# Optimization experiments

Measured on AMD Instinct MI355X. Metric: run time of the kernel, lower is better.

Reference implementation:

```python
import jax, jax.numpy as jnp
import numpy as np

K_SHARP = 10.0  # sigmoid sharpness from init kwarg k


def setup_inputs() -> dict:
    key = jax.random.key(0)
    k1, _ = jax.random.split(key)
    points = jax.random.normal(k1, (8192, 32), dtype=jnp.float32)
    # log-spaced thresholds, matching init_kwargs r_values
    r_values = jnp.asarray(np.logspace(0.0, np.log10(15.85), 16), dtype=jnp.float32)
    return {"points": points, "r_values": r_values}


def reference(points, r_values):
    n = points.shape[0]
    # pairwise euclidean distances (cdist p=2) via gram trick
    sq = jnp.sum(points * points, axis=-1)                       # [N]
    d2 = sq[:, None] + sq[None, :] - 2.0 * (points @ points.T)   # [N,N]
    d2 = jnp.maximum(d2, 0.0)
    iu = jnp.triu(jnp.ones((n, n), dtype=bool), k=1)             # strict upper triangle
    # safe sqrt: masked-out entries replaced by 1.0 (value irrelevant, avoids 0-grad issues)
    d = jnp.sqrt(jnp.where(iu, d2, 1.0))                         # [N,N]
    mask = iu & (d > 0.0)  # matches distances[distances > 0] after triu(1)
    cnt = jnp.sum(mask).astype(points.dtype)
    # one fused masked sigmoid-sum per threshold (sequential: one N*N temp at a time)
    sums = []
    for r in r_values:  # static length-16 loop over thresholds
        s = jnp.sum(jnp.where(mask, jax.nn.sigmoid(K_SHARP * (r - d)), 0.0))
        sums.append(s / cnt)
    correlation_sums = jnp.stack(sums)                           # [R]
    log_r = jnp.log(r_values)
    log_c = jnp.log(correlation_sums)
    A = jnp.stack([log_r, jnp.ones_like(log_r)], axis=1)         # [R,2]
    # full-rank least squares via normal equations (equivalent to lstsq here)
    sol = jnp.linalg.solve(A.T @ A, A.T @ log_c)                 # [slope, intercept]
    return -sol[0]
```

## Files before the change

kernel.cpp:

```cpp
#include <hip/hip_runtime.h>
#include <math.h>

#define NPTS 8192
#define DIM 32
#define TILE 128
#define NT (NPTS / TILE)
#define NTP (NT * (NT + 1) / 2)
#define NBINS 4096
#define BIN_SCALE 20.0f
#define NR 16
#define NBLK 512
#define LROW 40

using bf16x8 = __attribute__((ext_vector_type(8))) short;
using f32x4  = __attribute__((ext_vector_type(4))) float;

__device__ __forceinline__ unsigned short f2bf(float f) {
    unsigned u = __float_as_uint(f);
    return (unsigned short)((u + 0x7fffu + ((u >> 16) & 1u)) >> 16);
}

__global__ void k_prep(const float* __restrict__ pts, unsigned* __restrict__ bp,
                       float* __restrict__ sq, unsigned* __restrict__ cnt) {
    const int t = blockIdx.x * 256 + threadIdx.x;
    if (t < NBINS) cnt[t] = 0u;
    const int p = t >> 1, h = t & 1;
    const float4* src = (const float4*)(pts + (size_t)p * DIM + h * 16);
    const float4 v0 = src[0], v1 = src[1], v2 = src[2], v3 = src[3];
    float s = v0.x * v0.x + v0.y * v0.y + v0.z * v0.z + v0.w * v0.w
            + v1.x * v1.x + v1.y * v1.y + v1.z * v1.z + v1.w * v1.w
            + v2.x * v2.x + v2.y * v2.y + v2.z * v2.z + v2.w * v2.w
            + v3.x * v3.x + v3.y * v3.y + v3.z * v3.z + v3.w * v3.w;
    s += __shfl_xor(s, 1);
    if (!h) sq[p] = s;
    unsigned* dst = bp + (size_t)p * 16 + h * 8;
    dst[0] = (unsigned)f2bf(v0.x) | ((unsigned)f2bf(v0.y) << 16);
    dst[1] = (unsigned)f2bf(v0.z) | ((unsigned)f2bf(v0.w) << 16);
    dst[2] = (unsigned)f2bf(v1.x) | ((unsigned)f2bf(v1.y) << 16);
    dst[3] = (unsigned)f2bf(v1.z) | ((unsigned)f2bf(v1.w) << 16);
    dst[4] = (unsigned)f2bf(v2.x) | ((unsigned)f2bf(v2.y) << 16);
    dst[5] = (unsigned)f2bf(v2.z) | ((unsigned)f2bf(v2.w) << 16);
    dst[6] = (unsigned)f2bf(v3.x) | ((unsigned)f2bf(v3.y) << 16);
    dst[7] = (unsigned)f2bf(v3.z) | ((unsigned)f2bf(v3.w) << 16);
}


#define EPI1(ACC, SA, GROW, DIAGQ) { \
    const float d2_ = fmaf(-2.f, ACC, (SA) + sb); \
    const int bin_ = (int)fminf(fmaxf(d2_, 0.f) * BIN_SCALE, (float)(NBINS - 1)); \
    if (!(DIAGQ) || ((GROW) < gcol)) atomicAdd(&hist[bin_], 1u); }

#define TCLOOP(DIAGQ) \
    _Pragma("unroll") \
    for (int tc = 0; tc < 8; ++tc) { \
        const bf16x8 bf = *(const bf16x8*)&Bb[(tc * 16 + l15) * LROW + lc * 8]; \
        const f32x4 z = {0.f, 0.f, 0.f, 0.f}; \
        const f32x4 d0 = __builtin_amdgcn_mfma_f32_16x16x32_bf16(a0, bf, z, 0, 0, 0); \
        const f32x4 d1 = __builtin_amdgcn_mfma_f32_16x16x32_bf16(a1, bf, z, 0, 0, 0); \
        const float sb = sqb[tc * 16 + l15]; \
        const int gcol = tj * TILE + tc * 16 + l15; (void)gcol; \
        EPI1(d0[0], sa00, g0 + 0, DIAGQ) EPI1(d0[1], sa01, g0 + 1, DIAGQ) \
        EPI1(d0[2], sa02, g0 + 2, DIAGQ) EPI1(d0[3], sa03, g0 + 3, DIAGQ) \
        EPI1(d1[0], sa10, g1 + 0, DIAGQ) EPI1(d1[1], sa11, g1 + 1, DIAGQ) \
        EPI1(d1[2], sa12, g1 + 2, DIAGQ) EPI1(d1[3], sa13, g1 + 3, DIAGQ) \
    }

__global__ __launch_bounds__(256)
void k_hist(const uint4* __restrict__ bp4, const float* __restrict__ sq,
            unsigned* __restrict__ cnt) {
    __shared__ unsigned hist[NBINS];
    __shared__ unsigned short Ab[TILE * LROW];
    __shared__ unsigned short Bb[TILE * LROW];
    __shared__ float sqa[TILE], sqb[TILE];
    const int tid = threadIdx.x;
    const int lane = tid & 63, w = tid >> 6;
    const int l15 = lane & 15, lc = lane >> 4;
    for (int b = tid; b < NBINS; b += 256) hist[b] = 0u;
    const int P = gridDim.x;

    for (int tp = blockIdx.x; tp < NTP; tp += P) {
        int ti = 0, rr = tp;
        while (rr >= NT - ti) { rr -= NT - ti; ++ti; }
        const int tj = ti + rr;

        __syncthreads();
#pragma unroll
        for (int q = 0; q < 2; ++q) {
            const int g = tid + q * 256;
            const int p = g >> 2, c = g & 3;
            *(uint4*)&Ab[p * LROW + c * 8] = bp4[(size_t)ti * 512 + g];
            *(uint4*)&Bb[p * LROW + c * 8] = bp4[(size_t)tj * 512 + g];
        }
        if (tid < TILE) sqa[tid] = sq[ti * TILE + tid];
        else if (tid < 2 * TILE) sqb[tid - TILE] = sq[tj * TILE + (tid - TILE)];
        __syncthreads();

        const int r0 = (2 * w) * 16, r1 = r0 + 16;
        const bf16x8 a0 = *(const bf16x8*)&Ab[(r0 + l15) * LROW + lc * 8];
        const bf16x8 a1 = *(const bf16x8*)&Ab[(r1 + l15) * LROW + lc * 8];
        const float sa00 = sqa[r0 + lc * 4 + 0];
        const float sa01 = sqa[r0 + lc * 4 + 1];
        const float sa02 = sqa[r0 + lc * 4 + 2];
        const float sa03 = sqa[r0 + lc * 4 + 3];
        const float sa10 = sqa[r1 + lc * 4 + 0];
        const float sa11 = sqa[r1 + lc * 4 + 1];
        const float sa12 = sqa[r1 + lc * 4 + 2];
        const float sa13 = sqa[r1 + lc * 4 + 3];
        const int g0 = ti * TILE + r0 + lc * 4;
        const int g1 = ti * TILE + r1 + lc * 4;

        if (ti != tj) {
            TCLOOP(0)
        } else {
            TCLOOP(1)
        }
    }

    __syncthreads();
    for (int b = tid; b < NBINS; b += 256) {
        const unsigned h = hist[b];
        if (h) atomicAdd(&cnt[b], h);
    }
}

__global__ __launch_bounds__(1024)
void k_final(const unsigned* __restrict__ cnt, const float* __restrict__ rvals,
             float* __restrict__ out) {
    __shared__ double red[16][NR + 1];
    const int tid = threadIdx.x;
    float rv[NR];
#pragma unroll
    for (int t = 0; t < NR; ++t) rv[t] = rvals[t];

    double local[NR + 1];
#pragma unroll
    for (int t = 0; t <= NR; ++t) local[t] = 0.0;

#pragma unroll
    for (int q = 0; q < NBINS / 1024; ++q) {
        const int b = tid + q * 1024;
        const unsigned c = cnt[b];
        if (c) {
            const double cd = (double)c;
            local[NR] += cd;
            const float d = sqrtf(((float)b + 0.5f) / BIN_SCALE);
#pragma unroll
            for (int t = 0; t < NR; ++t) {
                const float x = 10.0f * (rv[t] - d);
                float s;
                if (x >= 0.f) s = 1.f / (1.f + __expf(-x));
                else          { const float e = __expf(x); s = e / (1.f + e); }
                local[t] += cd * (double)s;
            }
        }
    }

#pragma unroll
    for (int off = 32; off > 0; off >>= 1) {
#pragma unroll
        for (int t = 0; t <= NR; ++t)
            local[t] += __shfl_down(local[t], off);
    }
    const int wv = tid >> 6;
    if ((tid & 63) == 0) {
#pragma unroll
        for (int t = 0; t <= NR; ++t) red[wv][t] = local[t];
    }
    __syncthreads();

    if (tid == 0) {
        double sums[NR + 1];
#pragma unroll
        for (int t = 0; t <= NR; ++t) {
            double s = 0.0;
#pragma unroll
            for (int w2 = 0; w2 < 16; ++w2) s += red[w2][t];
            sums[t] = s;
        }
        const double cdn = sums[NR];
        double Sx = 0, Sy = 0, Sxx = 0, Sxy = 0;
#pragma unroll
        for (int t = 0; t < NR; ++t) {
            const double x = log((double)rv[t]);
            const double y = log(sums[t] / cdn);
            Sx += x; Sy += y; Sxx += x * x; Sxy += x * y;
        }
        const double R = (double)NR;
        const double slope = (R * Sxy - Sx * Sy) / (R * Sxx - Sx * Sx);
        out[0] = (float)(-slope);
    }
}

extern "C" void kernel_launch(void* const* d_in, const int* in_sizes, int n_in,
                              void* d_out, int out_size, void* d_ws, size_t ws_size,
                              hipStream_t stream) {
    const float* pts = (const float*)d_in[0];
    const float* rv  = (const float*)d_in[1];
    float* out = (float*)d_out;
    char* ws = (char*)d_ws;

    unsigned* bp = (unsigned*)ws;
    float* sq = (float*)(ws + 524288);
    unsigned* cnt = (unsigned*)(ws + 524288 + 32768);

    k_prep<<<64, 256, 0, stream>>>(pts, bp, sq, cnt);
    k_hist<<<NBLK, 256, 0, stream>>>((const uint4*)bp, sq, cnt);
    k_final<<<1, 1024, 0, stream>>>(cnt, rv, out);
}
```

Baseline: 60.42 us.

## Fuse final reduction into histogram kernel via last-block pattern and prescale norms

Removes the separate k_final launch by having the last block to finish k_hist (detected through an atomic counter at cnt[NBINS]) compute the sigmoid sums and slope. Squared norms are prescaled by the bin scale in k_prep so the epilogue saves a multiply. Grid size rises from 512 to 768 blocks. The tail work now runs on one 256-thread block instead of 1024 threads, and the added fences and atomics bring some extra cost.

```diff
diff --git a/kernel.cpp b/kernel.cpp
--- a/kernel.cpp
+++ b/kernel.cpp
@@ -9,7 +9,7 @@
 #define NBINS 4096
 #define BIN_SCALE 20.0f
 #define NR 16
-#define NBLK 512
+#define NBLK 768
 #define LROW 40
 
 using bf16x8 = __attribute__((ext_vector_type(8))) short;
@@ -21,9 +21,9 @@
 }
 
 __global__ void k_prep(const float* __restrict__ pts, unsigned* __restrict__ bp,
-                       float* __restrict__ sq, unsigned* __restrict__ cnt) {
+                       float* __restrict__ sq20, unsigned* __restrict__ cnt) {
     const int t = blockIdx.x * 256 + threadIdx.x;
-    if (t < NBINS) cnt[t] = 0u;
+    if (t <= NBINS) cnt[t] = 0u;
     const int p = t >> 1, h = t & 1;
     const float4* src = (const float4*)(pts + (size_t)p * DIM + h * 16);
     const float4 v0 = src[0], v1 = src[1], v2 = src[2], v3 = src[3];
@@ -32,7 +32,7 @@
             + v2.x * v2.x + v2.y * v2.y + v2.z * v2.z + v2.w * v2.w
             + v3.x * v3.x + v3.y * v3.y + v3.z * v3.z + v3.w * v3.w;
     s += __shfl_xor(s, 1);
-    if (!h) sq[p] = s;
+    if (!h) sq20[p] = s * BIN_SCALE;
     unsigned* dst = bp + (size_t)p * 16 + h * 8;
     dst[0] = (unsigned)f2bf(v0.x) | ((unsigned)f2bf(v0.y) << 16);
     dst[1] = (unsigned)f2bf(v0.z) | ((unsigned)f2bf(v0.w) << 16);
@@ -45,9 +45,9 @@
 }
 
 
-#define EPI1(ACC, SA, GROW, DIAGQ) { \
-    const float d2_ = fmaf(-2.f, ACC, (SA) + sb); \
-    const int bin_ = (int)fminf(fmaxf(d2_, 0.f) * BIN_SCALE, (float)(NBINS - 1)); \
+#define EPI1(ACC, SA20, GROW, DIAGQ) { \
+    const float bf_ = fmaf(-40.f, ACC, (SA20) + sb20); \
+    const int bin_ = (int)fminf(fmaxf(bf_, 0.f), (float)(NBINS - 1)); \
     if (!(DIAGQ) || ((GROW) < gcol)) atomicAdd(&hist[bin_], 1u); }
 
 #define TCLOOP(DIAGQ) \
@@ -57,7 +57,7 @@
         const f32x4 z = {0.f, 0.f, 0.f, 0.f}; \
         const f32x4 d0 = __builtin_amdgcn_mfma_f32_16x16x32_bf16(a0, bf, z, 0, 0, 0); \
         const f32x4 d1 = __builtin_amdgcn_mfma_f32_16x16x32_bf16(a1, bf, z, 0, 0, 0); \
-        const float sb = sqb[tc * 16 + l15]; \
+        const float sb20 = sqb[tc * 16 + l15]; \
         const int gcol = tj * TILE + tc * 16 + l15; (void)gcol; \
         EPI1(d0[0], sa00, g0 + 0, DIAGQ) EPI1(d0[1], sa01, g0 + 1, DIAGQ) \
         EPI1(d0[2], sa02, g0 + 2, DIAGQ) EPI1(d0[3], sa03, g0 + 3, DIAGQ) \
@@ -66,12 +66,15 @@
     }
 
 __global__ __launch_bounds__(256)
-void k_hist(const uint4* __restrict__ bp4, const float* __restrict__ sq,
-            unsigned* __restrict__ cnt) {
+void k_hist(const uint4* __restrict__ bp4, const float* __restrict__ sq20,
+            unsigned* __restrict__ cnt, const float* __restrict__ rvals,
+            float* __restrict__ out) {
     __shared__ unsigned hist[NBINS];
     __shared__ unsigned short Ab[TILE * LROW];
     __shared__ unsigned short Bb[TILE * LROW];
     __shared__ float sqa[TILE], sqb[TILE];
+    __shared__ double red[4][NR + 1];
+    __shared__ int amLast;
     const int tid = threadIdx.x;
     const int lane = tid & 63, w = tid >> 6;
     const int l15 = lane & 15, lc = lane >> 4;
@@ -91,8 +94,8 @@
             *(uint4*)&Ab[p * LROW + c * 8] = bp4[(size_t)ti * 512 + g];
             *(uint4*)&Bb[p * LROW + c * 8] = bp4[(size_t)tj * 512 + g];
         }
-        if (tid < TILE) sqa[tid] = sq[ti * TILE + tid];
-        else if (tid < 2 * TILE) sqb[tid - TILE] = sq[tj * TILE + (tid - TILE)];
+        if (tid < TILE) sqa[tid] = sq20[ti * TILE + tid];
+        else if (tid < 2 * TILE) sqb[tid - TILE] = sq20[tj * TILE + (tid - TILE)];
         __syncthreads();
 
         const int r0 = (2 * w) * 16, r1 = r0 + 16;
@@ -121,13 +124,14 @@
         const unsigned h = hist[b];
         if (h) atomicAdd(&cnt[b], h);
     }
-}
-
-__global__ __launch_bounds__(1024)
-void k_final(const unsigned* __restrict__ cnt, const float* __restrict__ rvals,
-             float* __restrict__ out) {
-    __shared__ double red[16][NR + 1];
-    const int tid = threadIdx.x;
+
+    __threadfence();
+    if (tid == 0)
+        amLast = (atomicAdd(&cnt[NBINS], 1u) == (unsigned)(gridDim.x - 1));
+    __syncthreads();
+    if (!amLast) return;
+    __threadfence();
+
     float rv[NR];
 #pragma unroll
     for (int t = 0; t < NR; ++t) rv[t] = rvals[t];
@@ -137,9 +141,9 @@
     for (int t = 0; t <= NR; ++t) local[t] = 0.0;
 
 #pragma unroll
-    for (int q = 0; q < NBINS / 1024; ++q) {
-        const int b = tid + q * 1024;
-        const unsigned c = cnt[b];
+    for (int q = 0; q < NBINS / 256; ++q) {
+        const int b = tid + q * 256;
+        const unsigned c = atomicAdd(&cnt[b], 0u);
         if (c) {
             const double cd = (double)c;
             local[NR] += cd;
@@ -161,22 +165,17 @@
         for (int t = 0; t <= NR; ++t)
             local[t] += __shfl_down(local[t], off);
     }
-    const int wv = tid >> 6;
     if ((tid & 63) == 0) {
 #pragma unroll
-        for (int t = 0; t <= NR; ++t) red[wv][t] = local[t];
+        for (int t = 0; t <= NR; ++t) red[w][t] = local[t];
     }
     __syncthreads();
 
     if (tid == 0) {
         double sums[NR + 1];
 #pragma unroll
-        for (int t = 0; t <= NR; ++t) {
-            double s = 0.0;
-#pragma unroll
-            for (int w2 = 0; w2 < 16; ++w2) s += red[w2][t];
-            sums[t] = s;
-        }
+        for (int t = 0; t <= NR; ++t)
+            sums[t] = red[0][t] + red[1][t] + red[2][t] + red[3][t];
         const double cdn = sums[NR];
         double Sx = 0, Sy = 0, Sxx = 0, Sxy = 0;
 #pragma unroll
@@ -200,10 +199,9 @@
     char* ws = (char*)d_ws;
 
     unsigned* bp = (unsigned*)ws;
-    float* sq = (float*)(ws + 524288);
+    float* sq20 = (float*)(ws + 524288);
     unsigned* cnt = (unsigned*)(ws + 524288 + 32768);
 
-    k_prep<<<64, 256, 0, stream>>>(pts, bp, sq, cnt);
-    k_hist<<<NBLK, 256, 0, stream>>>((const uint4*)bp, sq, cnt);
-    k_final<<<1, 1024, 0, stream>>>(cnt, rv, out);
-}
+    k_prep<<<64, 256, 0, stream>>>(pts, bp, sq20, cnt);
+    k_hist<<<NBLK, 256, 0, stream>>>((const uint4*)bp, sq20, cnt, rv, out);
+}
```

Measured after the change: 99.62 us. +64.9%, slower.
